# Kernel optimization log

Measured on AMD Instinct MI355X. Metric: run time of the kernel, lower is better.

## Reference

```python
import jax, jax.numpy as jnp
import numpy as np

B, T, D, S, K = 8, 4096, 1024, 64, 3
EPS = 1e-5

def setup_inputs() -> dict:
    key = jax.random.key(0)
    ks = jax.random.split(key, 10)
    def lin(k, out_d, in_d):
        s = 1.0 / np.sqrt(in_d)
        return jax.random.uniform(k, (out_d, in_d), jnp.float32, -s, s)
    return {
        "x": jax.random.normal(ks[0], (B, T, D), jnp.float32),
        "norm_w": jnp.ones((D,), jnp.float32),
        "norm_b": jnp.zeros((D,), jnp.float32),
        "in_w": lin(ks[1], 2 * D, D),
        "in_b": jnp.zeros((2 * D,), jnp.float32),
        "conv_w": jax.random.normal(ks[2], (D, 1, K), jnp.float32) / np.sqrt(K),
        "conv_b": jnp.zeros((D,), jnp.float32),
        "dt_w": lin(ks[3], S, D),
        "dt_b": jnp.zeros((S,), jnp.float32),
        "b_w": lin(ks[4], S, D),
        "b_b": jnp.zeros((S,), jnp.float32),
        "c_w": lin(ks[5], S, D),
        "c_b": jnp.zeros((S,), jnp.float32),
        "a_log": jax.random.normal(ks[6], (S,), jnp.float32) * 0.02,
        "d": jnp.ones((D,), jnp.float32),
        "out_w": lin(ks[7], D, D + S),
        "out_b": jnp.zeros((D,), jnp.float32),
    }

def reference(x, norm_w, norm_b, in_w, in_b, conv_w, conv_b,
              dt_w, dt_b, b_w, b_b, c_w, c_b, a_log, d, out_w, out_b):
    bsz, tlen, dim = x.shape
    sdim = a_log.shape[0]
    k = conv_w.shape[-1]
    residual = x
    # LayerNorm
    mu = jnp.mean(x, axis=-1, keepdims=True)
    var = jnp.mean(jnp.square(x - mu), axis=-1, keepdims=True)
    xn = (x - mu) * jax.lax.rsqrt(var + EPS) * norm_w + norm_b
    # in_proj and chunk
    h = xn @ in_w.T + in_b                       # (B,T,2D)
    x_proj, z = jnp.split(h, 2, axis=-1)         # each (B,T,D)
    # depthwise conv over time, 'same' padding
    xc = jax.lax.conv_general_dilated(
        x_proj.transpose(0, 2, 1), conv_w, (1,), [(k // 2, k // 2)],
        dimension_numbers=("NCH", "OIH", "NCH"), feature_group_count=dim)
    x_conv = jnp.tanh((xc + conv_b[None, :, None]).transpose(0, 2, 1))  # (B,T,D)
    # gate projections for all timesteps at once
    dt = jax.nn.softplus(z @ dt_w.T + dt_b) + 1e-4   # (B,T,S)
    b = jnp.tanh(z @ b_w.T + b_b)                    # (B,T,S)
    c = jnp.tanh(z @ c_w.T + c_b)                    # (B,T,S)
    a = -jnp.exp(a_log)                              # (S,)
    decay = jnp.exp(a * dt)                          # (B,T,S)
    # linear recurrence: state_t = state_{t-1} * decay_t + b_t
    def step(state, inp):
        dec_t, b_t = inp
        state = state * dec_t + b_t
        return state, state
    _, states = jax.lax.scan(step, jnp.zeros((bsz, sdim), x.dtype),
                             (decay.transpose(1, 0, 2), b.transpose(1, 0, 2)))
    states = states.transpose(1, 0, 2)               # (B,T,S)
    y = c * states
    mix = jnp.concatenate([x_conv * d, y], axis=-1)  # (B,T,D+S)
    out = mix @ out_w.T + out_b                      # (B,T,D)
    return residual + out
```

## Files before the change

kernel.cpp:

```cpp
#include <hip/hip_runtime.h>

#define TT 4096
#define DD 1024
#define NN 32768

typedef short s16x8 __attribute__((ext_vector_type(8)));
typedef float f32x4 __attribute__((ext_vector_type(4)));
typedef unsigned short ushort_t;

__device__ __forceinline__ unsigned short f2bf(float f) {
  unsigned u = __float_as_uint(f);
  u += 0x7FFFu + ((u >> 16) & 1u);
  return (unsigned short)(u >> 16);
}
__device__ __forceinline__ float bf2f(unsigned short h) {
  return __uint_as_float(((unsigned)h) << 16);
}
__device__ __forceinline__ void load_lds16(const void* g, void* l) {
  __builtin_amdgcn_global_load_lds(
      (const __attribute__((address_space(1))) unsigned int*)g,
      (__attribute__((address_space(3))) unsigned int*)l, 16, 0, 0);
}

__global__ __launch_bounds__(256)
void cvt_kernel(const float* __restrict__ s, ushort_t* __restrict__ d, int n) {
  int i = (blockIdx.x * 256 + threadIdx.x) * 4;
  if (i < n) {
    float4 v = *(const float4*)&s[i];
    ushort4 o; o.x = f2bf(v.x); o.y = f2bf(v.y); o.z = f2bf(v.z); o.w = f2bf(v.w);
    *(ushort4*)&d[i] = o;
  }
}

__global__ __launch_bounds__(256)
void w3pad_kernel(const float* __restrict__ dt_w, const float* __restrict__ b_w,
                  const float* __restrict__ c_w, ushort_t* __restrict__ w3) {
  int e = (blockIdx.x * 256 + threadIdx.x) * 4;
  int row = e >> 10, col = e & 1023;
  float4 v; v.x = 0.f; v.y = 0.f; v.z = 0.f; v.w = 0.f;
  if (row < 64)       v = *(const float4*)&dt_w[(row << 10) + col];
  else if (row < 128) v = *(const float4*)&b_w[((row - 64) << 10) + col];
  else if (row < 192) v = *(const float4*)&c_w[((row - 128) << 10) + col];
  ushort4 o; o.x = f2bf(v.x); o.y = f2bf(v.y); o.z = f2bf(v.z); o.w = f2bf(v.w);
  *(ushort4*)&w3[e] = o;
}

__global__ __launch_bounds__(256)
void tpose_kernel(const float* __restrict__ src, ushort_t* __restrict__ dst) {
  __shared__ float tile[64][65];
  int bx = blockIdx.x & 15, by = blockIdx.x >> 4;
  int tx = threadIdx.x & 63, ty0 = threadIdx.x >> 6;
  #pragma unroll
  for (int i = 0; i < 16; ++i) {
    int ty = ty0 * 16 + i;
    tile[ty][tx] = src[(size_t)(by * 64 + ty) * 1024 + bx * 64 + tx];
  }
  __syncthreads();
  #pragma unroll
  for (int i = 0; i < 16; ++i) {
    int ty = ty0 * 16 + i;
    dst[(size_t)(bx * 64 + ty) * 1024 + by * 64 + tx] = f2bf(tile[tx][ty]);
  }
}

__global__ void gbias_kernel(const float* __restrict__ dt_w, const float* __restrict__ b_w,
                             const float* __restrict__ c_w, const float* __restrict__ dt_b,
                             const float* __restrict__ b_b, const float* __restrict__ c_b,
                             const float* __restrict__ in_b, float* __restrict__ gb) {
  int i = blockIdx.x, lane = threadIdx.x;
  const float* wr = i < 64 ? dt_w + (size_t)i * 1024
                  : i < 128 ? b_w + (size_t)(i - 64) * 1024
                            : c_w + (size_t)(i - 128) * 1024;
  float s = 0.f;
  for (int j = lane; j < 1024; j += 64) s += wr[j] * in_b[1024 + j];
  #pragma unroll
  for (int off = 32; off; off >>= 1) s += __shfl_xor(s, off, 64);
  if (lane == 0) {
    float bb = i < 64 ? dt_b[i] : i < 128 ? b_b[i - 64] : c_b[i - 128];
    gb[i] = s + bb;
  }
}

__global__ __launch_bounds__(256)
void ln_kernel(const float* __restrict__ x, const float* __restrict__ w,
               const float* __restrict__ bv, ushort_t* __restrict__ xn)
{
  int row = blockIdx.x * 4 + (threadIdx.x >> 6);
  int lane = threadIdx.x & 63;
  const float* xr = x + (size_t)row * DD;
  float4 v[4];
  float s = 0.f, ss = 0.f;
  #pragma unroll
  for (int j = 0; j < 4; ++j) {
    v[j] = *(const float4*)&xr[j * 256 + lane * 4];
    s  += v[j].x + v[j].y + v[j].z + v[j].w;
    ss += v[j].x * v[j].x + v[j].y * v[j].y + v[j].z * v[j].z + v[j].w * v[j].w;
  }
  #pragma unroll
  for (int off = 32; off > 0; off >>= 1) {
    s  += __shfl_xor(s, off, 64);
    ss += __shfl_xor(ss, off, 64);
  }
  float mean = s * (1.f / 1024.f);
  float var  = ss * (1.f / 1024.f) - mean * mean;
  float rinv = rsqrtf(var + 1e-5f);
  #pragma unroll
  for (int j = 0; j < 4; ++j) {
    int c = j * 256 + lane * 4;
    float4 wv = *(const float4*)&w[c];
    float4 bb = *(const float4*)&bv[c];
    ushort4 o;
    o.x = f2bf((v[j].x - mean) * rinv * wv.x + bb.x);
    o.y = f2bf((v[j].y - mean) * rinv * wv.y + bb.y);
    o.z = f2bf((v[j].z - mean) * rinv * wv.z + bb.z);
    o.w = f2bf((v[j].w - mean) * rinv * wv.w + bb.w);
    *(ushort4*)&xn[(size_t)row * DD + c] = o;
  }
}

template<int EP>
__global__ __launch_bounds__(512, 2)
void gemm256(const ushort_t* __restrict__ A, const ushort_t* __restrict__ W,
             int M, int N, int K,
             const float* __restrict__ bias0,
             ushort_t* __restrict__ o0, ushort_t* __restrict__ o1)
{
  __shared__ ushort_t lds[65536];
  const int tid = threadIdx.x;
  const int lane = tid & 63;
  const int wid = tid >> 6;
  const int wr = wid >> 2;
  const int wc = wid & 3;
  const int lane15 = lane & 15;
  const int lgrp = lane >> 4;
  const int rsw = (lane15 & 7) << 4;
  const int ntn = N >> 8;
  int bid = blockIdx.x;
  { const int cpx = (int)gridDim.x >> 3; bid = (bid & 7) * cpx + (bid >> 3); }
  const int brow = (bid / ntn) << 8;
  const int bcol = (bid % ntn) << 8;
  const int nk = K >> 6;
  const int sRow = tid >> 3;
  const int sCol = (tid & 7) << 4;
  const char* ldsb = (const char*)lds;
  (void)M;

#define STG(bufb, isB, h, kt) do { \
    const int ktc_ = (kt) < nk ? (kt) : nk - 1; \
    const ushort_t* gsrc_ = (isB) ? W : A; \
    const int rowb_ = ((isB) ? bcol : brow) + (h) * 128; \
    _Pragma("unroll") \
    for (int j_ = 0; j_ < 2; ++j_) { \
      const int r_ = j_ * 64 + sRow; \
      load_lds16((const char*)(gsrc_ + (size_t)(rowb_ + r_) * K) + ktc_ * 128 + (sCol ^ ((r_ & 7) << 4)), \
                 (char*)lds + (bufb) * 65536 + (isB) * 32768 + (h) * 16384 + r_ * 128 + sCol); \
    } } while (0)

#define LDA_(bufb, m, kk) \
  (*(const s16x8*)(ldsb + (bufb) * 65536 + wr * 16384 + ((m) * 16 + lane15) * 128 + (((kk) * 64 + lgrp * 16) ^ rsw)))
#define LDB_(bufb, n, kk) \
  (*(const s16x8*)(ldsb + (bufb) * 65536 + 32768 + (wc >> 1) * 16384 + ((wc & 1) * 64 + (n) * 16 + lane15) * 128 + (((kk) * 64 + lgrp * 16) ^ rsw)))

#define BARR() asm volatile("s_barrier" ::: "memory")
#define VMW2() asm volatile("s_waitcnt vmcnt(2)" ::: "memory")
#define VMW4() asm volatile("s_waitcnt vmcnt(4)" ::: "memory")

#define RDA(dst, bufb, mh) do { \
    _Pragma("unroll") for (int kk = 0; kk < 2; ++kk) \
    _Pragma("unroll") for (int q = 0; q < 4; ++q) \
      dst[kk][q] = LDA_(bufb, (mh) * 4 + q, kk); } while (0)
#define RDB(dst, bufb, nh) do { \
    _Pragma("unroll") for (int kk = 0; kk < 2; ++kk) \
    _Pragma("unroll") for (int p = 0; p < 2; ++p) \
      dst[kk][p] = LDB_(bufb, (nh) * 2 + p, kk); } while (0)

#define MFMAQ(AF, BF, mh, nh) do { \
    __builtin_amdgcn_s_setprio(1); \
    _Pragma("unroll") for (int kk = 0; kk < 2; ++kk) \
    _Pragma("unroll") for (int q = 0; q < 4; ++q) \
    _Pragma("unroll") for (int p = 0; p < 2; ++p) \
      acc[(mh) * 4 + q][(nh) * 2 + p] = __builtin_amdgcn_mfma_f32_16x16x32_bf16( \
          AF[kk][q], BF[kk][p], acc[(mh) * 4 + q][(nh) * 2 + p], 0, 0, 0); \
    __builtin_amdgcn_s_setprio(0); } while (0)

  f32x4 acc[8][4];
  #pragma unroll
  for (int m = 0; m < 8; ++m) {
    #pragma unroll
    for (int n = 0; n < 4; ++n) acc[m][n] = (f32x4){0.f, 0.f, 0.f, 0.f};
  }
  s16x8 afP[2][4], afQ[2][4];
  s16x8 b0[2][2], b1[2][2];

  STG(0, 1, 0, 0); STG(0, 0, 0, 0); STG(0, 0, 1, 0); STG(0, 1, 1, 0);
  STG(1, 1, 0, 1); STG(1, 0, 0, 1);
  VMW4(); BARR();
  RDA(afP, 0, 0); RDB(b0, 0, 0);

  const int nIter = nk >> 1;
  for (int it = 0; it < nIter; ++it) {
    const int t0 = 2 * it;
    STG(1, 0, 1, t0 + 1);
    MFMAQ(afP, b0, 0, 0);
    RDB(b1, 0, 1); BARR();
    STG(1, 1, 1, t0 + 1);
    MFMAQ(afP, b1, 0, 1);
    RDA(afQ, 0, 1); BARR();
    STG(0, 1, 0, t0 + 2);
    MFMAQ(afQ, b1, 1, 1);
    VMW2(); BARR();
    STG(0, 0, 0, t0 + 2);
    MFMAQ(afQ, b0, 1, 0);
    RDA(afP, 1, 0); RDB(b1, 1, 1); BARR();
    STG(0, 0, 1, t0 + 2);
    MFMAQ(afP, b1, 0, 1);
    RDB(b0, 1, 0); BARR();
    STG(0, 1, 1, t0 + 2);
    MFMAQ(afP, b0, 0, 0);
    RDA(afQ, 1, 1); BARR();
    STG(1, 1, 0, t0 + 3);
    MFMAQ(afQ, b0, 1, 0);
    VMW2(); BARR();
    STG(1, 0, 0, t0 + 3);
    MFMAQ(afQ, b1, 1, 1);
    RDA(afP, 0, 0); RDB(b0, 0, 0); BARR();
  }
  if (nk & 1) {
    MFMAQ(afP, b0, 0, 0);
    RDB(b1, 0, 1);
    MFMAQ(afP, b1, 0, 1);
    RDA(afQ, 0, 1);
    MFMAQ(afQ, b1, 1, 1);
    MFMAQ(afQ, b0, 1, 0);
  }

#undef STG
#undef LDA_
#undef LDB_
#undef BARR
#undef VMW2
#undef VMW4
#undef RDA
#undef RDB
#undef MFMAQ

  #pragma unroll
  for (int m = 0; m < 8; ++m) {
    #pragma unroll
    for (int i = 0; i < 4; ++i) {
      const int r = brow + wr * 128 + m * 16 + lgrp * 4 + i;
      #pragma unroll
      for (int n = 0; n < 4; ++n) {
        const int col = bcol + wc * 64 + n * 16 + lane15;
        float v = acc[m][n][i] + bias0[col];
        if (col < DD) o0[(size_t)r * DD + col] = f2bf(v);
        else          o1[(size_t)r * DD + (col - DD)] = f2bf(v);
      }
    }
  }
}

__global__ __launch_bounds__(256, 2)
void gemm3_128(const ushort_t* __restrict__ A, const ushort_t* __restrict__ W,
               int M, int N, int K,
               const float* __restrict__ bias, const float* __restrict__ resid,
               float* __restrict__ outf)
{
  __shared__ ushort_t lds[32768];
  const int tid = threadIdx.x;
  const int lane = tid & 63;
  const int wid = tid >> 6;
  const int wr = wid >> 1;
  const int wc = wid & 1;
  const int lane15 = lane & 15;
  const int lgrp = lane >> 4;
  const int rsw = (lane15 & 7) << 4;
  const int ntn = N >> 7;
  int bid = blockIdx.x;
  { const int cpx = (int)gridDim.x >> 3; bid = (bid & 7) * cpx + (bid >> 3); }
  const int brow = (bid / ntn) << 7;
  const int bcol = (bid % ntn) << 7;
  const int nk = K >> 6;
  const int sRow = tid >> 3;
  const int sCol = (tid & 7) << 4;
  const char* ldsb = (const char*)lds;
  (void)M;

  f32x4 acc[4][4];
  #pragma unroll
  for (int q = 0; q < 4; ++q)
    #pragma unroll
    for (int p = 0; p < 4; ++p) acc[q][p] = (f32x4){0.f, 0.f, 0.f, 0.f};

#define STG3(bufb, kt) do { \
    _Pragma("unroll") \
    for (int j_ = 0; j_ < 4; ++j_) { \
      const int r_ = j_ * 32 + sRow; \
      load_lds16((const char*)(A + (size_t)(brow + r_) * K) + (kt) * 128 + (sCol ^ ((r_ & 7) << 4)), \
                 (char*)lds + (bufb) * 32768 + r_ * 128 + sCol); \
      load_lds16((const char*)(W + (size_t)(bcol + r_) * K) + (kt) * 128 + (sCol ^ ((r_ & 7) << 4)), \
                 (char*)lds + (bufb) * 32768 + 16384 + r_ * 128 + sCol); \
    } } while (0)

  STG3(0, 0);
  __syncthreads();

  int cur = 0;
  for (int t = 0; t < nk; ++t) {
    if (t + 1 < nk) STG3(cur ^ 1, t + 1);
    #pragma unroll
    for (int kk = 0; kk < 2; ++kk) {
      s16x8 af[4], bf[4];
      #pragma unroll
      for (int q = 0; q < 4; ++q)
        af[q] = *(const s16x8*)(ldsb + cur * 32768 +
                 (wr * 64 + q * 16 + lane15) * 128 + ((kk * 64 + lgrp * 16) ^ rsw));
      #pragma unroll
      for (int p = 0; p < 4; ++p)
        bf[p] = *(const s16x8*)(ldsb + cur * 32768 + 16384 +
                 (wc * 64 + p * 16 + lane15) * 128 + ((kk * 64 + lgrp * 16) ^ rsw));
      __builtin_amdgcn_s_setprio(1);
      #pragma unroll
      for (int q = 0; q < 4; ++q)
        #pragma unroll
        for (int p = 0; p < 4; ++p)
          acc[q][p] = __builtin_amdgcn_mfma_f32_16x16x32_bf16(af[q], bf[p], acc[q][p], 0, 0, 0);
      __builtin_amdgcn_s_setprio(0);
    }
    __syncthreads();
    cur ^= 1;
  }
#undef STG3

  #pragma unroll
  for (int q = 0; q < 4; ++q) {
    #pragma unroll
    for (int i = 0; i < 4; ++i) {
      const int r = brow + wr * 64 + q * 16 + lgrp * 4 + i;
      #pragma unroll
      for (int p = 0; p < 4; ++p) {
        const int col = bcol + wc * 64 + p * 16 + lane15;
        outf[(size_t)r * DD + col] = acc[q][p][i] + bias[col] + resid[(size_t)r * DD + col];
      }
    }
  }
}

__global__ __launch_bounds__(256)
void gemm128w(const ushort_t* __restrict__ A, const ushort_t* __restrict__ W,
              int M, int N, int K, ushort_t* __restrict__ o0)
{
  __shared__ ushort_t As[128 * 64];
  __shared__ ushort_t Bs[128 * 64];
  const int tid = threadIdx.x;
  const int lane = tid & 63;
  const int wid = tid >> 6;
  const int ntn = N >> 7;
  const int brow = (blockIdx.x / ntn) << 7;
  const int bcol = (blockIdx.x % ntn) << 7;
  const int wr = (wid >> 1) << 6;
  const int wc = (wid & 1) << 6;
  const int lane15 = lane & 15;
  const int lgrp = lane >> 4;
  (void)M;

  f32x4 acc[4][4];
  #pragma unroll
  for (int m = 0; m < 4; ++m)
    #pragma unroll
    for (int n = 0; n < 4; ++n)
      acc[m][n] = (f32x4){0.f, 0.f, 0.f, 0.f};

  const int r0 = tid >> 3;
  const int c0 = (tid & 7) << 3;
  const ushort_t* gA = A + (size_t)(brow + r0) * K + c0;
  const ushort_t* gW = W + (size_t)(bcol + r0) * K + c0;
  ushort_t* lA = &As[r0 * 64 + c0];
  ushort_t* lB = &Bs[r0 * 64 + c0];

  for (int k0 = 0; k0 < K; k0 += 64) {
    #pragma unroll
    for (int j = 0; j < 4; ++j) {
      load_lds16(gA + (size_t)(j * 32) * K + k0, lA + j * 32 * 64);
      load_lds16(gW + (size_t)(j * 32) * K + k0, lB + j * 32 * 64);
    }
    __syncthreads();
    #pragma unroll
    for (int kk = 0; kk < 2; ++kk) {
      s16x8 af[4], bfr[4];
      #pragma unroll
      for (int m = 0; m < 4; ++m)
        af[m] = *(const s16x8*)&As[(wr + m * 16 + lane15) * 64 + kk * 32 + lgrp * 8];
      #pragma unroll
      for (int n = 0; n < 4; ++n)
        bfr[n] = *(const s16x8*)&Bs[(wc + n * 16 + lane15) * 64 + kk * 32 + lgrp * 8];
      #pragma unroll
      for (int m = 0; m < 4; ++m)
        #pragma unroll
        for (int n = 0; n < 4; ++n)
          acc[m][n] = __builtin_amdgcn_mfma_f32_16x16x32_bf16(af[m], bfr[n], acc[m][n], 0, 0, 0);
    }
    __syncthreads();
  }

  #pragma unroll
  for (int m = 0; m < 4; ++m) {
    #pragma unroll
    for (int i = 0; i < 4; ++i) {
      const int r = brow + wr + m * 16 + lgrp * 4 + i;
      #pragma unroll
      for (int n = 0; n < 4; ++n) {
        const int col = bcol + wc + n * 16 + lane15;
        o0[(size_t)r * N + col] = f2bf(acc[m][n][i]);
      }
    }
  }
}

__global__ __launch_bounds__(256)
void gemm128g(const ushort_t* __restrict__ A, const ushort_t* __restrict__ W,
              int M, int N, int K,
              const float* __restrict__ gb, const float* __restrict__ alog,
              float* __restrict__ g0, float* __restrict__ g1, float* __restrict__ g2)
{
  __shared__ ushort_t As[128 * 64];
  __shared__ ushort_t Bs[128 * 64];
  const int tid = threadIdx.x;
  const int lane = tid & 63;
  const int wid = tid >> 6;
  const int ntn = N >> 7;
  const int brow = (blockIdx.x / ntn) << 7;
  const int bcol = (blockIdx.x % ntn) << 7;
  const int wr = (wid >> 1) << 6;
  const int wc = (wid & 1) << 6;
  const int lane15 = lane & 15;
  const int lgrp = lane >> 4;
  (void)M;

  f32x4 acc[4][4];
  #pragma unroll
  for (int m = 0; m < 4; ++m)
    #pragma unroll
    for (int n = 0; n < 4; ++n)
      acc[m][n] = (f32x4){0.f, 0.f, 0.f, 0.f};

  const int r0 = tid >> 3;
  const int c0 = (tid & 7) << 3;
  const ushort_t* gA = A + (size_t)(brow + r0) * K + c0;
  const ushort_t* gW = W + (size_t)(bcol + r0) * K + c0;
  ushort_t* lA = &As[r0 * 64 + c0];
  ushort_t* lB = &Bs[r0 * 64 + c0];

  for (int k0 = 0; k0 < K; k0 += 64) {
    #pragma unroll
    for (int j = 0; j < 4; ++j) {
      load_lds16(gA + (size_t)(j * 32) * K + k0, lA + j * 32 * 64);
      load_lds16(gW + (size_t)(j * 32) * K + k0, lB + j * 32 * 64);
    }
    __syncthreads();
    #pragma unroll
    for (int kk = 0; kk < 2; ++kk) {
      s16x8 af[4], bfr[4];
      #pragma unroll
      for (int m = 0; m < 4; ++m)
        af[m] = *(const s16x8*)&As[(wr + m * 16 + lane15) * 64 + kk * 32 + lgrp * 8];
      #pragma unroll
      for (int n = 0; n < 4; ++n)
        bfr[n] = *(const s16x8*)&Bs[(wc + n * 16 + lane15) * 64 + kk * 32 + lgrp * 8];
      #pragma unroll
      for (int m = 0; m < 4; ++m)
        #pragma unroll
        for (int n = 0; n < 4; ++n)
          acc[m][n] = __builtin_amdgcn_mfma_f32_16x16x32_bf16(af[m], bfr[n], acc[m][n], 0, 0, 0);
    }
    __syncthreads();
  }

  #pragma unroll
  for (int m = 0; m < 4; ++m) {
    #pragma unroll
    for (int i = 0; i < 4; ++i) {
      const int r = brow + wr + m * 16 + lgrp * 4 + i;
      #pragma unroll
      for (int n = 0; n < 4; ++n) {
        const int col = bcol + wc + n * 16 + lane15;
        float v = acc[m][n][i];
        if (col < 64) {
          float u = v + gb[col];
          float sp = (u > 20.f) ? u : log1pf(expf(u));
          g0[(size_t)r * 64 + col] = expf(-expf(alog[col]) * (sp + 1e-4f));
        } else if (col < 128) {
          g1[(size_t)r * 64 + (col - 64)] = tanhf(v + gb[col]);
        } else if (col < 192) {
          g2[(size_t)r * 64 + (col - 128)] = tanhf(v + gb[col]);
        }
      }
    }
  }
}

__global__ __launch_bounds__(256)
void conv_kernel(const ushort_t* __restrict__ xp, const float* __restrict__ cw,
                 const float* __restrict__ cb, const float* __restrict__ dvec,
                 ushort_t* __restrict__ mix)
{
  int idx = blockIdx.x * 256 + threadIdx.x;
  int row = idx >> 7;
  int d0 = (idx & 127) << 3;
  int t = row & (TT - 1);
  s16x8 cur = *(const s16x8*)&xp[(size_t)row * DD + d0];
  s16x8 prv; s16x8 nxt;
  #pragma unroll
  for (int j = 0; j < 8; ++j) { prv[j] = 0; nxt[j] = 0; }
  if (t > 0)      prv = *(const s16x8*)&xp[(size_t)(row - 1) * DD + d0];
  if (t < TT - 1) nxt = *(const s16x8*)&xp[(size_t)(row + 1) * DD + d0];
  float wv[24];
  #pragma unroll
  for (int j = 0; j < 6; ++j) *(float4*)&wv[j * 4] = *(const float4*)&cw[d0 * 3 + j * 4];
  float cbv[8], dv[8];
  *(float4*)&cbv[0] = *(const float4*)&cb[d0];
  *(float4*)&cbv[4] = *(const float4*)&cb[d0 + 4];
  *(float4*)&dv[0]  = *(const float4*)&dvec[d0];
  *(float4*)&dv[4]  = *(const float4*)&dvec[d0 + 4];
  s16x8 o;
  #pragma unroll
  for (int j = 0; j < 8; ++j) {
    float acc = cbv[j] + bf2f((ushort_t)prv[j]) * wv[j * 3]
              + bf2f((ushort_t)cur[j]) * wv[j * 3 + 1]
              + bf2f((ushort_t)nxt[j]) * wv[j * 3 + 2];
    o[j] = (short)f2bf(tanhf(acc) * dv[j]);
  }
  *(s16x8*)&mix[(size_t)row * 1088 + d0] = o;
}

__global__ void scanA_kernel(const float* __restrict__ dec, const float* __restrict__ bb,
                             float* __restrict__ P, float* __restrict__ Q)
{
  int b = blockIdx.x >> 6, ci = blockIdx.x & 63, s = threadIdx.x;
  size_t base = (((size_t)b * TT) + ci * 64) * 64 + s;
  float p = 1.f, q = 0.f;
  #pragma unroll 4
  for (int t = 0; t < 64; ++t) {
    float d = dec[base + (size_t)t * 64];
    float w = bb[base + (size_t)t * 64];
    q = q * d + w; p *= d;
  }
  int o = (b * 64 + ci) * 64 + s;
  P[o] = p; Q[o] = q;
}

__global__ void scanB_kernel(const float* __restrict__ P, const float* __restrict__ Q,
                             float* __restrict__ I)
{
  int b = blockIdx.x, s = threadIdx.x;
  float st = 0.f;
  for (int ci = 0; ci < 64; ++ci) {
    int o = (b * 64 + ci) * 64 + s;
    I[o] = st;
    st = st * P[o] + Q[o];
  }
}

__global__ void scanC_kernel(const float* __restrict__ dec, const float* __restrict__ bb,
                             const float* __restrict__ cc, const float* __restrict__ I,
                             ushort_t* __restrict__ mix)
{
  int b = blockIdx.x >> 6, ci = blockIdx.x & 63, s = threadIdx.x;
  size_t base = (((size_t)b * TT) + ci * 64) * 64 + s;
  float st = I[(b * 64 + ci) * 64 + s];
  size_t mrow = (size_t)b * TT + ci * 64;
  #pragma unroll 4
  for (int t = 0; t < 64; ++t) {
    size_t o = base + (size_t)t * 64;
    st = st * dec[o] + bb[o];
    mix[(mrow + t) * 1088 + 1024 + s] = (ushort_t)f2bf(cc[o] * st);
  }
}

extern "C" void kernel_launch(void* const* d_in, const int* in_sizes, int n_in,
                              void* d_out, int out_size, void* d_ws, size_t ws_size,
                              hipStream_t stream)
{
  (void)in_sizes; (void)n_in; (void)out_size; (void)ws_size;
  const float* x      = (const float*)d_in[0];
  const float* norm_w = (const float*)d_in[1];
  const float* norm_b = (const float*)d_in[2];
  const float* in_w   = (const float*)d_in[3];
  const float* in_b   = (const float*)d_in[4];
  const float* conv_w = (const float*)d_in[5];
  const float* conv_b = (const float*)d_in[6];
  const float* dt_w   = (const float*)d_in[7];
  const float* dt_b   = (const float*)d_in[8];
  const float* b_w    = (const float*)d_in[9];
  const float* b_b    = (const float*)d_in[10];
  const float* c_w    = (const float*)d_in[11];
  const float* c_b    = (const float*)d_in[12];
  const float* a_log  = (const float*)d_in[13];
  const float* dvec   = (const float*)d_in[14];
  const float* out_w  = (const float*)d_in[15];
  const float* out_b  = (const float*)d_in[16];
  float* out = (float*)d_out;

  char* p = (char*)d_ws;
  ushort_t* mix    = (ushort_t*)p;
  ushort_t* xn     = mix;
  p += 71303168;
  ushort_t* xproj  = (ushort_t*)p; p += 67108864;
  char*     zreg   = p;            p += 67108864;
  ushort_t* w1_bf  = (ushort_t*)p; p += 4194304;
  ushort_t* w3     = (ushort_t*)p; p += 524288;
  ushort_t* outw_bf= (ushort_t*)p; p += 2228224;
  float* P = (float*)p; p += 131072;
  float* Q = (float*)p; p += 131072;
  float* I = (float*)p; p += 131072;

  float* gdec = (float*)zreg;
  float* gbb  = (float*)(zreg + 8388608);
  float* gcc  = (float*)(zreg + 16777216);
  ushort_t* inw2t  = (ushort_t*)(zreg + 33554432);
  float*    gb     = (float*)(zreg + 37748736);
  ushort_t* wgates = (ushort_t*)(zreg + 41943040);

  cvt_kernel<<<1024, 256, 0, stream>>>(in_w, w1_bf, 1048576);
  cvt_kernel<<<1088, 256, 0, stream>>>(out_w, outw_bf, 1114112);
  tpose_kernel<<<256, 256, 0, stream>>>(in_w + 1048576, inw2t);
  w3pad_kernel<<<256, 256, 0, stream>>>(dt_w, b_w, c_w, w3);
  gemm128w<<<16, 256, 0, stream>>>(w3, inw2t, 256, 1024, 1024, wgates);
  gbias_kernel<<<192, 64, 0, stream>>>(dt_w, b_w, c_w, dt_b, b_b, c_b, in_b, gb);

  ln_kernel<<<8192, 256, 0, stream>>>(x, norm_w, norm_b, xn);

  gemm256<0><<<(NN / 256) * (1024 / 256), 512, 0, stream>>>(
      xn, w1_bf, NN, 1024, 1024, in_b, xproj, nullptr);

  gemm128g<<<(NN / 128) * (256 / 128), 256, 0, stream>>>(
      xn, wgates, NN, 256, 1024, gb, a_log, gdec, gbb, gcc);

  conv_kernel<<<NN * 128 / 256, 256, 0, stream>>>(xproj, conv_w, conv_b, dvec, mix);

  scanA_kernel<<<512, 64, 0, stream>>>(gdec, gbb, P, Q);
  scanB_kernel<<<8, 64, 0, stream>>>(P, Q, I);
  scanC_kernel<<<512, 64, 0, stream>>>(gdec, gbb, gcc, I, mix);

  gemm3_128<<<(NN / 128) * (1024 / 128), 256, 0, stream>>>(
      mix, outw_bf, NN, 1024, 1088, out_b, x, out);
}
```

Measured before the change: 392.7 us.

## Shrink out-proj GEMM tile to 64x128, prefetch residual, batch scanB loads

The output projection GEMM now uses 64x128 tiles with four waves split along columns, smaller LDS and three blocks per CU. This doubles the grid size for better occupancy and load balance. Residual values are prefetched into registers four k-steps before the end, hiding their load latency behind MFMA work. scanB also loads all P/Q values up front so the serial recurrence does not wait on memory. The tradeoff is less reuse per tile, which doubles W reads, plus higher register pressure from the 32-float residual buffer.

```diff
diff --git a/kernel.cpp b/kernel.cpp
--- a/kernel.cpp
+++ b/kernel.cpp
@@ -260,46 +260,49 @@
   }
 }
 
-__global__ __launch_bounds__(256, 2)
-void gemm3_128(const ushort_t* __restrict__ A, const ushort_t* __restrict__ W,
-               int M, int N, int K,
-               const float* __restrict__ bias, const float* __restrict__ resid,
-               float* __restrict__ outf)
-{
-  __shared__ ushort_t lds[32768];
+__global__ __launch_bounds__(256, 3)
+void gemm3_64(const ushort_t* __restrict__ A, const ushort_t* __restrict__ W,
+              int M, int N, int K,
+              const float* __restrict__ bias, const float* __restrict__ resid,
+              float* __restrict__ outf)
+{
+  __shared__ ushort_t lds[24576];
   const int tid = threadIdx.x;
   const int lane = tid & 63;
-  const int wid = tid >> 6;
-  const int wr = wid >> 1;
-  const int wc = wid & 1;
+  const int wc = tid >> 6;
   const int lane15 = lane & 15;
   const int lgrp = lane >> 4;
   const int rsw = (lane15 & 7) << 4;
   const int ntn = N >> 7;
   int bid = blockIdx.x;
   { const int cpx = (int)gridDim.x >> 3; bid = (bid & 7) * cpx + (bid >> 3); }
-  const int brow = (bid / ntn) << 7;
+  const int brow = (bid / ntn) << 6;
   const int bcol = (bid % ntn) << 7;
   const int nk = K >> 6;
-  const int sRow = tid >> 3;
-  const int sCol = (tid & 7) << 4;
+  const int sR = tid >> 3;
+  const int sC = (tid & 7) << 4;
   const char* ldsb = (const char*)lds;
   (void)M;
 
-  f32x4 acc[4][4];
+  f32x4 acc[4][2];
   #pragma unroll
   for (int q = 0; q < 4; ++q)
     #pragma unroll
-    for (int p = 0; p < 4; ++p) acc[q][p] = (f32x4){0.f, 0.f, 0.f, 0.f};
+    for (int p = 0; p < 2; ++p) acc[q][p] = (f32x4){0.f, 0.f, 0.f, 0.f};
+  float rs[32];
 
 #define STG3(bufb, kt) do { \
     _Pragma("unroll") \
+    for (int j_ = 0; j_ < 2; ++j_) { \
+      const int r_ = j_ * 32 + sR; \
+      load_lds16((const char*)(A + (size_t)(brow + r_) * K) + (kt) * 128 + (sC ^ ((r_ & 7) << 4)), \
+                 (char*)lds + (bufb) * 24576 + r_ * 128 + sC); \
+    } \
+    _Pragma("unroll") \
     for (int j_ = 0; j_ < 4; ++j_) { \
-      const int r_ = j_ * 32 + sRow; \
-      load_lds16((const char*)(A + (size_t)(brow + r_) * K) + (kt) * 128 + (sCol ^ ((r_ & 7) << 4)), \
-                 (char*)lds + (bufb) * 32768 + r_ * 128 + sCol); \
-      load_lds16((const char*)(W + (size_t)(bcol + r_) * K) + (kt) * 128 + (sCol ^ ((r_ & 7) << 4)), \
-                 (char*)lds + (bufb) * 32768 + 16384 + r_ * 128 + sCol); \
+      const int r_ = j_ * 32 + sR; \
+      load_lds16((const char*)(W + (size_t)(bcol + r_) * K) + (kt) * 128 + (sC ^ ((r_ & 7) << 4)), \
+                 (char*)lds + (bufb) * 24576 + 8192 + r_ * 128 + sC); \
     } } while (0)
 
   STG3(0, 0);
@@ -308,22 +311,32 @@
   int cur = 0;
   for (int t = 0; t < nk; ++t) {
     if (t + 1 < nk) STG3(cur ^ 1, t + 1);
-    #pragma unroll
-    for (int kk = 0; kk < 2; ++kk) {
-      s16x8 af[4], bf[4];
-      #pragma unroll
-      for (int q = 0; q < 4; ++q)
-        af[q] = *(const s16x8*)(ldsb + cur * 32768 +
-                 (wr * 64 + q * 16 + lane15) * 128 + ((kk * 64 + lgrp * 16) ^ rsw));
-      #pragma unroll
-      for (int p = 0; p < 4; ++p)
-        bf[p] = *(const s16x8*)(ldsb + cur * 32768 + 16384 +
-                 (wc * 64 + p * 16 + lane15) * 128 + ((kk * 64 + lgrp * 16) ^ rsw));
-      __builtin_amdgcn_s_setprio(1);
+    if (t == nk - 4) {
       #pragma unroll
       for (int q = 0; q < 4; ++q)
         #pragma unroll
-        for (int p = 0; p < 4; ++p)
+        for (int p = 0; p < 2; ++p)
+          #pragma unroll
+          for (int i = 0; i < 4; ++i)
+            rs[q * 8 + p * 4 + i] =
+              resid[(size_t)(brow + q * 16 + lgrp * 4 + i) * DD + bcol + wc * 32 + p * 16 + lane15];
+    }
+    #pragma unroll
+    for (int kk = 0; kk < 2; ++kk) {
+      s16x8 af[4], bf[2];
+      #pragma unroll
+      for (int q = 0; q < 4; ++q)
+        af[q] = *(const s16x8*)(ldsb + cur * 24576 +
+                 (q * 16 + lane15) * 128 + ((kk * 64 + lgrp * 16) ^ rsw));
+      #pragma unroll
+      for (int p = 0; p < 2; ++p)
+        bf[p] = *(const s16x8*)(ldsb + cur * 24576 + 8192 +
+                 (wc * 32 + p * 16 + lane15) * 128 + ((kk * 64 + lgrp * 16) ^ rsw));
+      __builtin_amdgcn_s_setprio(1);
+      #pragma unroll
+      for (int q = 0; q < 4; ++q)
+        #pragma unroll
+        for (int p = 0; p < 2; ++p)
           acc[q][p] = __builtin_amdgcn_mfma_f32_16x16x32_bf16(af[q], bf[p], acc[q][p], 0, 0, 0);
       __builtin_amdgcn_s_setprio(0);
     }
@@ -336,11 +349,11 @@
   for (int q = 0; q < 4; ++q) {
     #pragma unroll
     for (int i = 0; i < 4; ++i) {
-      const int r = brow + wr * 64 + q * 16 + lgrp * 4 + i;
-      #pragma unroll
-      for (int p = 0; p < 4; ++p) {
-        const int col = bcol + wc * 64 + p * 16 + lane15;
-        outf[(size_t)r * DD + col] = acc[q][p][i] + bias[col] + resid[(size_t)r * DD + col];
+      const int r = brow + q * 16 + lgrp * 4 + i;
+      #pragma unroll
+      for (int p = 0; p < 2; ++p) {
+        const int col = bcol + wc * 32 + p * 16 + lane15;
+        outf[(size_t)r * DD + col] = acc[q][p][i] + bias[col] + rs[q * 8 + p * 4 + i];
       }
     }
   }
@@ -553,11 +566,18 @@
                              float* __restrict__ I)
 {
   int b = blockIdx.x, s = threadIdx.x;
+  float pv[64], qv[64];
+  #pragma unroll
+  for (int ci = 0; ci < 64; ++ci) {
+    int o = (b * 64 + ci) * 64 + s;
+    pv[ci] = P[o]; qv[ci] = Q[o];
+  }
   float st = 0.f;
+  #pragma unroll
   for (int ci = 0; ci < 64; ++ci) {
     int o = (b * 64 + ci) * 64 + s;
     I[o] = st;
-    st = st * P[o] + Q[o];
+    st = st * pv[ci] + qv[ci];
   }
 }
 
@@ -642,6 +662,6 @@
   scanB_kernel<<<8, 64, 0, stream>>>(P, Q, I);
   scanC_kernel<<<512, 64, 0, stream>>>(gdec, gbb, gcc, I, mix);
 
-  gemm3_128<<<(NN / 128) * (1024 / 128), 256, 0, stream>>>(
+  gemm3_64<<<(NN / 64) * (1024 / 128), 256, 0, stream>>>(
       mix, outw_bf, NN, 1024, 1088, out_b, x, out);
 }
```

Result: slower. 404.9 us (+3.1%).
